# Kernel optimization log

Measured on AMD Instinct MI355X. Metric: run time of the kernel, lower is better.

Reference implementation:

```python
import jax, jax.numpy as jnp
import numpy as np

EPS = 1e-10
TEMP = 1.0


def setup_inputs() -> dict:
    key = jax.random.key(0)
    ks = jax.random.split(key, 8)
    num_nodes, embed_dim, hidden_dim, num_edges = 50000, 128, 64, 600000
    node_embed = jax.random.normal(ks[0], (num_nodes, embed_dim), dtype=jnp.float32)
    edge_index = jax.random.randint(ks[1], (2, num_edges), 0, num_nodes, dtype=jnp.int64)
    u1 = jax.random.uniform(ks[2], (num_edges,), dtype=jnp.float32)
    u2 = jax.random.uniform(ks[3], (num_edges,), dtype=jnp.float32)
    # Linear weights (kaiming-ish scale)
    W1 = jax.random.normal(ks[4], (2 * embed_dim, hidden_dim), dtype=jnp.float32) * (1.0 / np.sqrt(2 * embed_dim))
    b1 = jnp.zeros((hidden_dim,), dtype=jnp.float32)
    W2 = jax.random.normal(ks[5], (hidden_dim, 1), dtype=jnp.float32) * (1.0 / np.sqrt(hidden_dim))
    b2 = jnp.zeros((1,), dtype=jnp.float32)
    return {"node_embed": node_embed, "edge_index": edge_index, "u1": u1, "u2": u2,
            "W1": W1, "b1": b1, "W2": W2, "b2": b2}


def reference(node_embed, edge_index, u1, u2, W1, b1, W2, b2):
    row, col = edge_index[0], edge_index[1]
    # gather + concat: [num_edges, 2*embed_dim]
    edge_feat = jnp.concatenate([node_embed[row], node_embed[col]], axis=1)
    # small MLP (dropout is identity in eval)
    h = jax.nn.relu(edge_feat @ W1 + b1)
    edge_logits = (h @ W2 + b2).squeeze(-1)  # [num_edges]
    # Gumbel-sigmoid (soft)
    g1 = -jnp.log(-jnp.log(jnp.clip(u1, EPS, 1.0 - EPS)))
    g2 = -jnp.log(-jnp.log(jnp.clip(u2, EPS, 1.0 - EPS)))
    edge_probs = jax.nn.sigmoid((edge_logits + g1 - g2) / TEMP)
    return edge_probs
```

## Files before the change

kernel.cpp:

```cpp
#include <hip/hip_runtime.h>
#include <stdint.h>

typedef float  floatx4 __attribute__((ext_vector_type(4)));
typedef short  short8  __attribute__((ext_vector_type(8)));
typedef float  f4v     __attribute__((ext_vector_type(4)));
typedef unsigned int uint32;

#define GS_EPS 1e-10f

__device__ __forceinline__ unsigned short f2bf(float x) {
  uint32 u = __float_as_uint(x);
  u += 0x7FFFu + ((u >> 16) & 1u);
  return (unsigned short)(u >> 16);
}

__global__ void conv_nodes_kernel(const float* __restrict__ src,
                                  unsigned short* __restrict__ dst, int n8) {
  int i = blockIdx.x * 256 + threadIdx.x;
  if (i < n8) {
    f4v v0 = *(const f4v*)(src + (size_t)i * 8);
    f4v v1 = *(const f4v*)(src + (size_t)i * 8 + 4);
    short8 t;
    t[0] = (short)f2bf(v0[0]); t[1] = (short)f2bf(v0[1]);
    t[2] = (short)f2bf(v0[2]); t[3] = (short)f2bf(v0[3]);
    t[4] = (short)f2bf(v1[0]); t[5] = (short)f2bf(v1[1]);
    t[6] = (short)f2bf(v1[2]); t[7] = (short)f2bf(v1[3]);
    *(short8*)(dst + (size_t)i * 8) = t;
  }
}

__global__ void conv_w1_kernel(const float* __restrict__ W1,
                               unsigned short* __restrict__ w1blk) {
  int i = blockIdx.x * 256 + threadIdx.x;
  int chunk = i >> 6;
  int n = i & 63;
  uint32 d[4];
#pragma unroll
  for (int j = 0; j < 4; ++j) {
    unsigned short lo = f2bf(W1[(chunk * 8 + 2 * j) * 64 + n]);
    unsigned short hi = f2bf(W1[(chunk * 8 + 2 * j + 1) * 64 + n]);
    d[j] = (uint32)lo | ((uint32)hi << 16);
  }
  *(uint32*)&w1blk[(size_t)i * 8 + 0] = d[0];
  *(uint32*)&w1blk[(size_t)i * 8 + 2] = d[1];
  *(uint32*)&w1blk[(size_t)i * 8 + 4] = d[2];
  *(uint32*)&w1blk[(size_t)i * 8 + 6] = d[3];
}

__global__ __launch_bounds__(512, 8) void edge_mlp_kernel(
    const unsigned short* __restrict__ node_bf16,
    const unsigned short* __restrict__ w1g,
    const int* __restrict__ ei,
    const float* __restrict__ u1, const float* __restrict__ u2,
    const float* __restrict__ b1, const float* __restrict__ W2,
    const float* __restrict__ b2,
    float* __restrict__ out, int num_edges) {
  __shared__ __align__(16) unsigned short w1blk[32 * 64 * 8];

  const int tid = threadIdx.x;
  const int wave = tid >> 6;
  const int lane = tid & 63;
  const int q = lane >> 4;
  const int l16 = lane & 15;
  const int wavebase = blockIdx.x * 128 + wave * 16;

#pragma unroll
  for (int it = 0; it < 4; ++it) {
    int idx = it * 512 + tid;
    short8 v = *(const short8*)(w1g + (size_t)idx * 8);
    *(short8*)&w1blk[(size_t)idx * 8] = v;
  }

  int el = wavebase + lane;
  if (el > num_edges - 1) el = num_edges - 1;
  unsigned long long oddmask = __ballot(ei[2 * el + 1] != 0);
  const bool idx64 = (oddmask == 0ULL);

  int e = wavebase + l16;
  if (e > num_edges - 1) e = num_edges - 1;
  int nr, nc;
  if (idx64) {
    nr = ei[2 * e];
    nc = ei[2 * (num_edges + e)];
  } else {
    nr = ei[e];
    nc = ei[num_edges + e];
  }

  short8 af[8];
  {
    const unsigned short* pr = node_bf16 + (size_t)nr * 128 + q * 8;
    const unsigned short* pc = node_bf16 + (size_t)nc * 128 + q * 8;
#pragma unroll
    for (int kk = 0; kk < 4; ++kk) af[kk] = *(const short8*)(pr + kk * 32);
#pragma unroll
    for (int kk = 0; kk < 4; ++kk) af[4 + kk] = *(const short8*)(pc + kk * 32);
  }

  __syncthreads();

  floatx4 acc[4];
#pragma unroll
  for (int nn = 0; nn < 4; ++nn) {
    floatx4 z = {0.f, 0.f, 0.f, 0.f};
    acc[nn] = z;
  }

#pragma unroll
  for (int kk = 0; kk < 8; ++kk) {
#pragma unroll
    for (int nn = 0; nn < 4; ++nn) {
      short8 bf = *(const short8*)&w1blk[(size_t)((kk * 4 + q) * 64 + nn * 16 + l16) * 8];
      acc[nn] = __builtin_amdgcn_mfma_f32_16x16x32_bf16(af[kk], bf, acc[nn], 0, 0, 0);
    }
  }

  float p0 = 0.f, p1 = 0.f, p2 = 0.f, p3 = 0.f;
#pragma unroll
  for (int nn = 0; nn < 4; ++nn) {
    float bb = b1[nn * 16 + l16];
    float ww = W2[nn * 16 + l16];
    floatx4 a = acc[nn];
    p0 += fmaxf(a[0] + bb, 0.f) * ww;
    p1 += fmaxf(a[1] + bb, 0.f) * ww;
    p2 += fmaxf(a[2] + bb, 0.f) * ww;
    p3 += fmaxf(a[3] + bb, 0.f) * ww;
  }
#pragma unroll
  for (int s = 1; s < 16; s <<= 1) {
    p0 += __shfl_xor(p0, s, 64);
    p1 += __shfl_xor(p1, s, 64);
    p2 += __shfl_xor(p2, s, 64);
    p3 += __shfl_xor(p3, s, 64);
  }
  if (l16 < 4) {
    float logit = (l16 == 0) ? p0 : (l16 == 1) ? p1 : (l16 == 2) ? p2 : p3;
    logit += b2[0];
    int eo = wavebase + q * 4 + l16;
    if (eo < num_edges) {
      float a1 = fminf(fmaxf(u1[eo], GS_EPS), 1.0f);
      float a2 = fminf(fmaxf(u2[eo], GS_EPS), 1.0f);
      float g1 = -__logf(-__logf(a1));
      float g2 = -__logf(-__logf(a2));
      float x = logit + g1 - g2;
      out[eo] = 1.f / (1.f + __expf(-x));
    }
  }
}

extern "C" void kernel_launch(void* const* d_in, const int* in_sizes, int n_in,
                              void* d_out, int out_size, void* d_ws, size_t ws_size,
                              hipStream_t stream) {
  const float* node_embed = (const float*)d_in[0];
  const int* ei = (const int*)d_in[1];
  const float* u1 = (const float*)d_in[2];
  const float* u2 = (const float*)d_in[3];
  const float* W1 = (const float*)d_in[4];
  const float* b1 = (const float*)d_in[5];
  const float* W2 = (const float*)d_in[6];
  const float* b2 = (const float*)d_in[7];
  float* out = (float*)d_out;

  const int num_edges = in_sizes[2];
  const int num_nodes = in_sizes[0] / 128;

  unsigned short* node_bf16 = (unsigned short*)d_ws;
  const size_t node_tbl_bytes = (size_t)num_nodes * 128 * sizeof(unsigned short);
  unsigned short* w1blk = (unsigned short*)((char*)d_ws + ((node_tbl_bytes + 15) & ~(size_t)15));

  int n8 = (num_nodes * 128) / 8;
  conv_nodes_kernel<<<(n8 + 255) / 256, 256, 0, stream>>>(node_embed, node_bf16, n8);
  conv_w1_kernel<<<8, 256, 0, stream>>>(W1, w1blk);

  const int nblocks = (num_edges + 127) / 128;
  edge_mlp_kernel<<<nblocks, 512, 0, stream>>>(
      node_bf16, w1blk, ei, u1, u2, b1, W2, b2, out, num_edges);
}
```

Before: 135.7 us.

## Precompute per-node projections through W1 halves, gather them per edge

Because the first linear layer is applied to a concatenation of two node embeddings, it is split into per-node projections: each node is multiplied by both halves of W1 once (50k nodes instead of 600k edges), with the bias folded into the row half, and the result is stored in bf16. The edge kernel then gathers two 64-wide bf16 projection rows per edge, adds them, applies ReLU and the W2 dot product with shuffle reductions. This removes roughly an order of magnitude of MFMA work and the shared-memory weight staging per edge block, but it adds an extra bf16 rounding of the pre-activation sums.

```diff
diff --git a/kernel.cpp b/kernel.cpp
--- a/kernel.cpp
+++ b/kernel.cpp
@@ -13,56 +13,39 @@
   u += 0x7FFFu + ((u >> 16) & 1u);
   return (unsigned short)(u >> 16);
 }
-
-__global__ void conv_nodes_kernel(const float* __restrict__ src,
-                                  unsigned short* __restrict__ dst, int n8) {
-  int i = blockIdx.x * 256 + threadIdx.x;
-  if (i < n8) {
-    f4v v0 = *(const f4v*)(src + (size_t)i * 8);
-    f4v v1 = *(const f4v*)(src + (size_t)i * 8 + 4);
-    short8 t;
-    t[0] = (short)f2bf(v0[0]); t[1] = (short)f2bf(v0[1]);
-    t[2] = (short)f2bf(v0[2]); t[3] = (short)f2bf(v0[3]);
-    t[4] = (short)f2bf(v1[0]); t[5] = (short)f2bf(v1[1]);
-    t[6] = (short)f2bf(v1[2]); t[7] = (short)f2bf(v1[3]);
-    *(short8*)(dst + (size_t)i * 8) = t;
-  }
+__device__ __forceinline__ float bf2f(short v) {
+  return __uint_as_float(((uint32)(unsigned short)v) << 16);
 }
 
-__global__ void conv_w1_kernel(const float* __restrict__ W1,
-                               unsigned short* __restrict__ w1blk) {
+__global__ void conv_w1cat_kernel(const float* __restrict__ W1,
+                                  unsigned short* __restrict__ w1g) {
   int i = blockIdx.x * 256 + threadIdx.x;
-  int chunk = i >> 6;
-  int n = i & 63;
+  int chunk = i >> 7;
+  int n = i & 127;
+  const float* src = (n < 64) ? (W1 + n) : (W1 + 128 * 64 + (n - 64));
   uint32 d[4];
 #pragma unroll
   for (int j = 0; j < 4; ++j) {
-    unsigned short lo = f2bf(W1[(chunk * 8 + 2 * j) * 64 + n]);
-    unsigned short hi = f2bf(W1[(chunk * 8 + 2 * j + 1) * 64 + n]);
+    int k0 = chunk * 8 + 2 * j;
+    unsigned short lo = f2bf(src[(size_t)k0 * 64]);
+    unsigned short hi = f2bf(src[(size_t)(k0 + 1) * 64]);
     d[j] = (uint32)lo | ((uint32)hi << 16);
   }
-  *(uint32*)&w1blk[(size_t)i * 8 + 0] = d[0];
-  *(uint32*)&w1blk[(size_t)i * 8 + 2] = d[1];
-  *(uint32*)&w1blk[(size_t)i * 8 + 4] = d[2];
-  *(uint32*)&w1blk[(size_t)i * 8 + 6] = d[3];
+#pragma unroll
+  for (int j = 0; j < 4; ++j) *(uint32*)&w1g[(size_t)i * 8 + 2 * j] = d[j];
 }
 
-__global__ __launch_bounds__(512, 8) void edge_mlp_kernel(
-    const unsigned short* __restrict__ node_bf16,
-    const unsigned short* __restrict__ w1g,
-    const int* __restrict__ ei,
-    const float* __restrict__ u1, const float* __restrict__ u2,
-    const float* __restrict__ b1, const float* __restrict__ W2,
-    const float* __restrict__ b2,
-    float* __restrict__ out, int num_edges) {
-  __shared__ __align__(16) unsigned short w1blk[32 * 64 * 8];
+__global__ __launch_bounds__(512, 4) void pcompute_kernel(
+    const float* __restrict__ E, const unsigned short* __restrict__ w1g,
+    const float* __restrict__ b1, unsigned short* __restrict__ P,
+    int num_nodes) {
+  __shared__ __align__(16) unsigned short w1blk[16 * 128 * 8];
 
   const int tid = threadIdx.x;
   const int wave = tid >> 6;
   const int lane = tid & 63;
   const int q = lane >> 4;
   const int l16 = lane & 15;
-  const int wavebase = blockIdx.x * 128 + wave * 16;
 
 #pragma unroll
   for (int it = 0; it < 4; ++it) {
@@ -71,79 +54,119 @@
     *(short8*)&w1blk[(size_t)idx * 8] = v;
   }
 
-  int el = wavebase + lane;
+  const int rowbase = blockIdx.x * 128 + wave * 16;
+  int row = rowbase + l16;
+  const bool ok = row < num_nodes;
+  if (!ok) row = num_nodes - 1;
+
+  short8 bfr[4];
+#pragma unroll
+  for (int kk = 0; kk < 4; ++kk) {
+    const float* p = E + (size_t)row * 128 + kk * 32 + q * 8;
+    f4v v0 = *(const f4v*)p;
+    f4v v1 = *(const f4v*)(p + 4);
+    short8 t;
+    t[0] = (short)f2bf(v0[0]); t[1] = (short)f2bf(v0[1]);
+    t[2] = (short)f2bf(v0[2]); t[3] = (short)f2bf(v0[3]);
+    t[4] = (short)f2bf(v1[0]); t[5] = (short)f2bf(v1[1]);
+    t[6] = (short)f2bf(v1[2]); t[7] = (short)f2bf(v1[3]);
+    bfr[kk] = t;
+  }
+  __syncthreads();
+
+  floatx4 acc[8];
+#pragma unroll
+  for (int t = 0; t < 8; ++t) {
+    floatx4 z = {0.f, 0.f, 0.f, 0.f};
+    acc[t] = z;
+  }
+#pragma unroll
+  for (int kk = 0; kk < 4; ++kk) {
+#pragma unroll
+    for (int t = 0; t < 8; ++t) {
+      short8 af = *(const short8*)&w1blk[(size_t)((kk * 4 + q) * 128 + t * 16 + l16) * 8];
+      acc[t] = __builtin_amdgcn_mfma_f32_16x16x32_bf16(af, bfr[kk], acc[t], 0, 0, 0);
+    }
+  }
+
+#pragma unroll
+  for (int t = 0; t < 8; ++t) {
+    floatx4 a = acc[t];
+    if (t < 4) {
+      f4v bv = *(const f4v*)(b1 + t * 16 + q * 4);
+      a[0] += bv[0]; a[1] += bv[1]; a[2] += bv[2]; a[3] += bv[3];
+    }
+    uint32 lo = (uint32)f2bf(a[0]) | ((uint32)f2bf(a[1]) << 16);
+    uint32 hi = (uint32)f2bf(a[2]) | ((uint32)f2bf(a[3]) << 16);
+    if (ok) {
+      uint32* dst = (uint32*)(P + (size_t)(rowbase + l16) * 128 + t * 16 + q * 4);
+      dst[0] = lo;
+      dst[1] = hi;
+    }
+  }
+}
+
+__global__ __launch_bounds__(256, 8) void edge_kernel(
+    const unsigned short* __restrict__ P,
+    const int* __restrict__ ei,
+    const float* __restrict__ u1, const float* __restrict__ u2,
+    const float* __restrict__ W2, const float* __restrict__ b2,
+    float* __restrict__ out, int num_edges) {
+  const int tid = threadIdx.x;
+  const int wave = tid >> 6;
+  const int lane = tid & 63;
+  const int g = lane >> 3;
+  const int h = lane & 7;
+  const int wbase = blockIdx.x * 128 + wave * 32;
+
+  f4v w0 = *(const f4v*)(W2 + h * 8);
+  f4v w1v = *(const f4v*)(W2 + h * 8 + 4);
+  const float bias2 = b2[0];
+
+  int el = wbase + (lane & 31);
   if (el > num_edges - 1) el = num_edges - 1;
   unsigned long long oddmask = __ballot(ei[2 * el + 1] != 0);
   const bool idx64 = (oddmask == 0ULL);
-
-  int e = wavebase + l16;
-  if (e > num_edges - 1) e = num_edges - 1;
-  int nr, nc;
+  int eR, eC;
   if (idx64) {
-    nr = ei[2 * e];
-    nc = ei[2 * (num_edges + e)];
+    eR = ei[2 * el];
+    eC = ei[2 * (num_edges + el)];
   } else {
-    nr = ei[e];
-    nc = ei[num_edges + e];
+    eR = ei[el];
+    eC = ei[num_edges + el];
   }
 
-  short8 af[8];
-  {
-    const unsigned short* pr = node_bf16 + (size_t)nr * 128 + q * 8;
-    const unsigned short* pc = node_bf16 + (size_t)nc * 128 + q * 8;
+  short8 ar[4], ac[4];
 #pragma unroll
-    for (int kk = 0; kk < 4; ++kk) af[kk] = *(const short8*)(pr + kk * 32);
-#pragma unroll
-    for (int kk = 0; kk < 4; ++kk) af[4 + kk] = *(const short8*)(pc + kk * 32);
-  }
-
-  __syncthreads();
-
-  floatx4 acc[4];
-#pragma unroll
-  for (int nn = 0; nn < 4; ++nn) {
-    floatx4 z = {0.f, 0.f, 0.f, 0.f};
-    acc[nn] = z;
+  for (int s = 0; s < 4; ++s) {
+    int nr = __shfl(eR, s * 8 + g, 64);
+    int nc = __shfl(eC, s * 8 + g, 64);
+    ar[s] = *(const short8*)(P + (size_t)nr * 128 + h * 8);
+    ac[s] = *(const short8*)(P + (size_t)nc * 128 + 64 + h * 8);
   }
 
 #pragma unroll
-  for (int kk = 0; kk < 8; ++kk) {
+  for (int s = 0; s < 4; ++s) {
+    float acc = 0.f;
 #pragma unroll
-    for (int nn = 0; nn < 4; ++nn) {
-      short8 bf = *(const short8*)&w1blk[(size_t)((kk * 4 + q) * 64 + nn * 16 + l16) * 8];
-      acc[nn] = __builtin_amdgcn_mfma_f32_16x16x32_bf16(af[kk], bf, acc[nn], 0, 0, 0);
+    for (int j = 0; j < 8; ++j) {
+      float hv = fmaxf(bf2f(ar[s][j]) + bf2f(ac[s][j]), 0.f);
+      float ww = (j < 4) ? w0[j] : w1v[j - 4];
+      acc = fmaf(hv, ww, acc);
     }
-  }
-
-  float p0 = 0.f, p1 = 0.f, p2 = 0.f, p3 = 0.f;
-#pragma unroll
-  for (int nn = 0; nn < 4; ++nn) {
-    float bb = b1[nn * 16 + l16];
-    float ww = W2[nn * 16 + l16];
-    floatx4 a = acc[nn];
-    p0 += fmaxf(a[0] + bb, 0.f) * ww;
-    p1 += fmaxf(a[1] + bb, 0.f) * ww;
-    p2 += fmaxf(a[2] + bb, 0.f) * ww;
-    p3 += fmaxf(a[3] + bb, 0.f) * ww;
-  }
-#pragma unroll
-  for (int s = 1; s < 16; s <<= 1) {
-    p0 += __shfl_xor(p0, s, 64);
-    p1 += __shfl_xor(p1, s, 64);
-    p2 += __shfl_xor(p2, s, 64);
-    p3 += __shfl_xor(p3, s, 64);
-  }
-  if (l16 < 4) {
-    float logit = (l16 == 0) ? p0 : (l16 == 1) ? p1 : (l16 == 2) ? p2 : p3;
-    logit += b2[0];
-    int eo = wavebase + q * 4 + l16;
-    if (eo < num_edges) {
-      float a1 = fminf(fmaxf(u1[eo], GS_EPS), 1.0f);
-      float a2 = fminf(fmaxf(u2[eo], GS_EPS), 1.0f);
-      float g1 = -__logf(-__logf(a1));
-      float g2 = -__logf(-__logf(a2));
-      float x = logit + g1 - g2;
-      out[eo] = 1.f / (1.f + __expf(-x));
+    acc += __shfl_xor(acc, 1, 64);
+    acc += __shfl_xor(acc, 2, 64);
+    acc += __shfl_xor(acc, 4, 64);
+    if (h == 0) {
+      int e = wbase + s * 8 + g;
+      if (e < num_edges) {
+        float a1 = fminf(fmaxf(u1[e], GS_EPS), 1.0f);
+        float a2 = fminf(fmaxf(u2[e], GS_EPS), 1.0f);
+        float g1 = -__logf(-__logf(a1));
+        float g2 = -__logf(-__logf(a2));
+        float x = acc + bias2 + g1 - g2;
+        out[e] = 1.f / (1.f + __expf(-x));
+      }
     }
   }
 }
@@ -164,15 +187,13 @@
   const int num_edges = in_sizes[2];
   const int num_nodes = in_sizes[0] / 128;
 
-  unsigned short* node_bf16 = (unsigned short*)d_ws;
-  const size_t node_tbl_bytes = (size_t)num_nodes * 128 * sizeof(unsigned short);
-  unsigned short* w1blk = (unsigned short*)((char*)d_ws + ((node_tbl_bytes + 15) & ~(size_t)15));
+  unsigned short* P = (unsigned short*)d_ws;
+  const size_t p_bytes = (size_t)num_nodes * 128 * sizeof(unsigned short);
+  unsigned short* w1g = (unsigned short*)((char*)d_ws + ((p_bytes + 255) & ~(size_t)255));
 
-  int n8 = (num_nodes * 128) / 8;
-  conv_nodes_kernel<<<(n8 + 255) / 256, 256, 0, stream>>>(node_embed, node_bf16, n8);
-  conv_w1_kernel<<<8, 256, 0, stream>>>(W1, w1blk);
-
-  const int nblocks = (num_edges + 127) / 128;
-  edge_mlp_kernel<<<nblocks, 512, 0, stream>>>(
-      node_bf16, w1blk, ei, u1, u2, b1, W2, b2, out, num_edges);
+  conv_w1cat_kernel<<<8, 256, 0, stream>>>(W1, w1g);
+  const int pblocks = (num_nodes + 127) / 128;
+  pcompute_kernel<<<pblocks, 512, 0, stream>>>(node_embed, w1g, b1, P, num_nodes);
+  const int eblocks = (num_edges + 127) / 128;
+  edge_kernel<<<eblocks, 256, 0, stream>>>(P, ei, u1, u2, W2, b2, out, num_edges);
 }
```

After: 116.1 us. 1.17x faster.
